# Performance work log

Hardware: AMD Instinct MI355X
Metric: run time of the kernel (lower is better)

## Reference

```python
import jax, jax.numpy as jnp
import numpy as np

N, D, F, E, K = 8192, 1024, 4096, 8, 2


def setup_inputs() -> dict:
    key = jax.random.key(0)
    ks = jax.random.split(key, 4)
    x = jax.random.normal(ks[0], (N, D), dtype=jnp.float32)
    Wg = jax.random.normal(ks[1], (D, E), dtype=jnp.float32) * 0.02
    W1 = jax.random.normal(ks[2], (E, D, F), dtype=jnp.float32) * 0.02
    b1 = jnp.zeros((E, F), dtype=jnp.float32)
    W2 = jax.random.normal(ks[3], (E, F, D), dtype=jnp.float32) * 0.02
    b2 = jnp.zeros((E, D), dtype=jnp.float32)
    return {"x": x, "Wg": Wg, "W1": W1, "b1": b1, "W2": W2, "b2": b2}


def reference(x, Wg, W1, b1, W2, b2):
    # Top-k softmax gate (TopKGate): pick K experts per token, renormalize.
    logits = x @ Wg                                        # [N, E]
    probs = jax.nn.softmax(logits, axis=-1)
    gate_vals, expert_idx = jax.lax.top_k(probs, K)        # [N, K]
    gate_w = gate_vals / jnp.sum(gate_vals, axis=-1, keepdims=True)

    # Expert FFN (dispatch/combine math): the torch code sorts tokens by expert
    # id, all-to-alls them to the owning rank, applies the local Expert MLP,
    # and combines back weighted by gate_w. The jit-friendly equivalent is to
    # compute every expert's MLP for all tokens and gather the selected rows.
    h = jax.nn.relu(jnp.einsum('nd,edf->enf', x, W1) + b1[:, None, :])  # [E, N, F]
    o = jnp.einsum('enf,efd->end', h, W2) + b2[:, None, :]               # [E, N, D]

    tok = jnp.arange(x.shape[0])
    sel = o[expert_idx, tok[:, None]]                      # [N, K, D]
    y = jnp.sum(gate_w[..., None] * sel, axis=1)           # [N, D]
    return y
```

## Files before the change

### kernel.cpp

```cpp
#include <hip/hip_runtime.h>

#define N_TOK 8192
#define DIM   1024
#define FFN   4096
#define NEXP  8
#define TOPK  2
#define NENT  (N_TOK * TOPK)
#define MAXM  20

using short8  = __attribute__((ext_vector_type(8))) short;
using floatx4 = __attribute__((ext_vector_type(4))) float;

__device__ __forceinline__ unsigned short f2bf(float f) {
    union { float f; unsigned u; } v; v.f = f;
    unsigned r = v.u + 0x7fffu + ((v.u >> 16) & 1u);
    return (unsigned short)(r >> 16);
}

#define GLOAD_LDS16(gptr, lptr) __builtin_amdgcn_global_load_lds( \
    (__attribute__((address_space(1))) void*)(void*)(gptr),       \
    (__attribute__((address_space(3))) void*)(lptr), 16, 0, 0)


__global__ __launch_bounds__(256) void cvt_x_kernel(const float4* __restrict__ in,
                                                    ushort4* __restrict__ out) {
    int i = blockIdx.x * 256 + threadIdx.x;
    float4 v = in[i];
    ushort4 o;
    o.x = f2bf(v.x); o.y = f2bf(v.y); o.z = f2bf(v.z); o.w = f2bf(v.w);
    out[i] = o;
}

__global__ __launch_bounds__(256) void transpose_cvt(const float* __restrict__ in,
                                                     unsigned short* __restrict__ out,
                                                     int R, int C) {
    __shared__ float tile[64][65];
    int e  = blockIdx.z;
    int c0 = blockIdx.x * 64;
    int r0 = blockIdx.y * 64;
    const float* inp = in + (size_t)e * R * C;
    unsigned short* outp = out + (size_t)e * R * C;
    int tid = threadIdx.x;
    int lrow = tid >> 6, lcol = tid & 63;
#pragma unroll
    for (int i = 0; i < 16; i++) {
        int r = i * 4 + lrow;
        tile[r][lcol] = inp[(size_t)(r0 + r) * C + c0 + lcol];
    }
    __syncthreads();
    int r4 = (tid & 15) * 4;
#pragma unroll
    for (int i = 0; i < 4; i++) {
        int c = i * 16 + (tid >> 4);
        ushort4 o;
        o.x = f2bf(tile[r4 + 0][c]);
        o.y = f2bf(tile[r4 + 1][c]);
        o.z = f2bf(tile[r4 + 2][c]);
        o.w = f2bf(tile[r4 + 3][c]);
        *(ushort4*)&outp[(size_t)(c0 + c) * R + r0 + r4] = o;
    }
}


__global__ __launch_bounds__(256) void gating_kernel(const float* __restrict__ x,
                                                     const float* __restrict__ wg,
                                                     int* __restrict__ topk_e,
                                                     float* __restrict__ topk_w,
                                                     int* __restrict__ counts) {
    int wave = threadIdx.x >> 6, lane = threadIdx.x & 63;
    int t = blockIdx.x * 4 + wave;
    const float* xr = x + (size_t)t * DIM;
    float acc[NEXP];
#pragma unroll
    for (int e = 0; e < NEXP; e++) acc[e] = 0.f;
    for (int it = 0; it < DIM / 64; it++) {
        int d = it * 64 + lane;
        float xv = xr[d];
        const float4* wr = (const float4*)(wg + d * NEXP);
        float4 w0 = wr[0], w1 = wr[1];
        acc[0] += xv * w0.x; acc[1] += xv * w0.y; acc[2] += xv * w0.z; acc[3] += xv * w0.w;
        acc[4] += xv * w1.x; acc[5] += xv * w1.y; acc[6] += xv * w1.z; acc[7] += xv * w1.w;
    }
#pragma unroll
    for (int e = 0; e < NEXP; e++) {
#pragma unroll
        for (int off = 32; off > 0; off >>= 1) acc[e] += __shfl_xor(acc[e], off);
    }
    if (lane == 0) {
        int e1 = 0; float l1 = acc[0];
        for (int e = 1; e < NEXP; e++) if (acc[e] > l1) { l1 = acc[e]; e1 = e; }
        int e2 = -1; float l2 = -3.4e38f;
        for (int e = 0; e < NEXP; e++) if (e != e1 && acc[e] > l2) { l2 = acc[e]; e2 = e; }
        float w1v = 1.f / (1.f + expf(l2 - l1));
        topk_e[t * 2]     = e1;  topk_e[t * 2 + 1] = e2;
        topk_w[t * 2]     = w1v; topk_w[t * 2 + 1] = 1.f - w1v;
        atomicAdd(&counts[e1], 1);
        atomicAdd(&counts[e2], 1);
    }
}

__global__ void prefix_kernel(const int* __restrict__ counts, int* __restrict__ offs) {
    if (threadIdx.x == 0) {
        int s = 0;
        for (int e = 0; e < NEXP; e++) { offs[e] = s; s += counts[e]; }
        offs[NEXP] = s;
    }
}

__global__ __launch_bounds__(256) void scatter_kernel(const int* __restrict__ topk_e,
                                                      const float* __restrict__ topk_w,
                                                      const int* __restrict__ offs,
                                                      int* __restrict__ cursors,
                                                      int* __restrict__ entry_token,
                                                      float* __restrict__ entry_wgt) {
    int t = blockIdx.x * 256 + threadIdx.x;
#pragma unroll
    for (int k = 0; k < TOPK; k++) {
        int e = topk_e[t * 2 + k];
        int pos = offs[e] + atomicAdd(&cursors[e], 1);
        entry_token[pos] = t;
        entry_wgt[pos]  = topk_w[t * 2 + k];
    }
}


__global__ __launch_bounds__(256) void gemm1_kernel(
    const unsigned short* __restrict__ xb,
    const unsigned short* __restrict__ w1t,
    const float* __restrict__ b1,
    const int* __restrict__ offs,
    const int* __restrict__ entry_token,
    unsigned short* __restrict__ h)
{
    int bid  = blockIdx.x;
    int e    = bid & 7;
    int grp  = bid % (8 * MAXM);
    int mt   = grp >> 3;
    int nt   = bid / (8 * MAXM);
    int base = offs[e];
    int cnt  = offs[e + 1] - base;
    int m0   = mt * 128;
    if (m0 >= cnt) return;
    int f0   = nt * 128;

    __shared__ unsigned short As[128 * 32];
    __shared__ unsigned short Bs[128 * 32];
    __shared__ int toks[128];

    int tid = threadIdx.x;
    if (tid < 128) {
        int r = m0 + tid;
        toks[tid] = entry_token[base + (r < cnt ? r : 0)];
    }
    __syncthreads();

    int wave = tid >> 6, lane = tid & 63;
    int wm = (wave >> 1) * 64, wn = (wave & 1) * 64;

    int lr = lane >> 2, sl = lane & 3;
    int g0 = (sl ^ ((lr >> 1) & 3)) * 8;
    const unsigned short* aG[2];
    const unsigned short* bG[2];
    unsigned short* ldsA[2];
    unsigned short* ldsB[2];
#pragma unroll
    for (int c = 0; c < 2; c++) {
        int row = wave * 32 + c * 16 + lr;
        aG[c] = xb + (size_t)toks[row] * DIM + g0;
        bG[c] = w1t + ((size_t)e * FFN + f0 + row) * DIM + g0;
        ldsA[c] = &As[(wave * 32 + c * 16) * 32];
        ldsB[c] = &Bs[(wave * 32 + c * 16) * 32];
    }

    floatx4 acc[4][4];
#pragma unroll
    for (int i = 0; i < 4; i++)
#pragma unroll
        for (int j = 0; j < 4; j++) acc[i][j] = (floatx4)0.f;

    int quad = lane >> 4, rm = lane & 15;
    int slf  = (quad ^ ((rm >> 1) & 3)) * 8;
    int arow = (wm + rm) * 32;
    int brow = (wn + rm) * 32;

    for (int kk = 0; kk < DIM / 32; kk++) {
        GLOAD_LDS16(aG[0], ldsA[0]);
        GLOAD_LDS16(aG[1], ldsA[1]);
        GLOAD_LDS16(bG[0], ldsB[0]);
        GLOAD_LDS16(bG[1], ldsB[1]);
        aG[0] += 32; aG[1] += 32; bG[0] += 32; bG[1] += 32;
        __syncthreads();
        short8 af[4], bfr[4];
#pragma unroll
        for (int mi = 0; mi < 4; mi++) af[mi] = *(const short8*)&As[arow + mi * 512 + slf];
#pragma unroll
        for (int ni = 0; ni < 4; ni++) bfr[ni] = *(const short8*)&Bs[brow + ni * 512 + slf];
#pragma unroll
        for (int mi = 0; mi < 4; mi++)
#pragma unroll
            for (int ni = 0; ni < 4; ni++)
                acc[mi][ni] = __builtin_amdgcn_mfma_f32_16x16x32_bf16(af[mi], bfr[ni], acc[mi][ni], 0, 0, 0);
        __syncthreads();
    }

#pragma unroll
    for (int mi = 0; mi < 4; mi++) {
        int mbase = wm + mi * 16 + quad * 4;
#pragma unroll
        for (int ni = 0; ni < 4; ni++) {
            int f = f0 + wn + ni * 16 + rm;
            float bias = b1[e * FFN + f];
            floatx4 v = acc[mi][ni];
#pragma unroll
            for (int r = 0; r < 4; r++) {
                int row = m0 + mbase + r;
                if (row < cnt) {
                    float t = v[r] + bias;
                    t = t > 0.f ? t : 0.f;
                    h[(size_t)(base + row) * FFN + f] = f2bf(t);
                }
            }
        }
    }
}


__global__ __launch_bounds__(256) void gemm2_kernel(
    const unsigned short* __restrict__ h,
    const unsigned short* __restrict__ w2t,
    const float* __restrict__ b2,
    const int* __restrict__ offs,
    const int* __restrict__ entry_token,
    const float* __restrict__ entry_wgt,
    float* __restrict__ y)
{
    int bid  = blockIdx.x;
    int e    = bid & 7;
    int grp  = bid % (8 * MAXM);
    int mt   = grp >> 3;
    int nt   = bid / (8 * MAXM);
    int base = offs[e];
    int cnt  = offs[e + 1] - base;
    int m0   = mt * 128;
    if (m0 >= cnt) return;
    int n0   = nt * 128;

    __shared__ unsigned short As[128 * 32];
    __shared__ unsigned short Bs[128 * 32];

    int tid = threadIdx.x;
    int wave = tid >> 6, lane = tid & 63;
    int wm = (wave >> 1) * 64, wn = (wave & 1) * 64;

    int lr = lane >> 2, sl = lane & 3;
    int g0 = (sl ^ ((lr >> 1) & 3)) * 8;
    const unsigned short* aG[2];
    const unsigned short* bG[2];
    unsigned short* ldsA[2];
    unsigned short* ldsB[2];
#pragma unroll
    for (int c = 0; c < 2; c++) {
        int row = wave * 32 + c * 16 + lr;
        aG[c] = h + (size_t)(base + m0 + row) * FFN + g0;
        bG[c] = w2t + ((size_t)e * DIM + n0 + row) * FFN + g0;
        ldsA[c] = &As[(wave * 32 + c * 16) * 32];
        ldsB[c] = &Bs[(wave * 32 + c * 16) * 32];
    }

    floatx4 acc[4][4];
#pragma unroll
    for (int i = 0; i < 4; i++)
#pragma unroll
        for (int j = 0; j < 4; j++) acc[i][j] = (floatx4)0.f;

    int quad = lane >> 4, rm = lane & 15;
    int slf  = (quad ^ ((rm >> 1) & 3)) * 8;
    int arow = (wm + rm) * 32;
    int brow = (wn + rm) * 32;

    for (int kk = 0; kk < FFN / 32; kk++) {
        GLOAD_LDS16(aG[0], ldsA[0]);
        GLOAD_LDS16(aG[1], ldsA[1]);
        GLOAD_LDS16(bG[0], ldsB[0]);
        GLOAD_LDS16(bG[1], ldsB[1]);
        aG[0] += 32; aG[1] += 32; bG[0] += 32; bG[1] += 32;
        __syncthreads();
        short8 af[4], bfr[4];
#pragma unroll
        for (int mi = 0; mi < 4; mi++) af[mi] = *(const short8*)&As[arow + mi * 512 + slf];
#pragma unroll
        for (int ni = 0; ni < 4; ni++) bfr[ni] = *(const short8*)&Bs[brow + ni * 512 + slf];
#pragma unroll
        for (int mi = 0; mi < 4; mi++)
#pragma unroll
            for (int ni = 0; ni < 4; ni++)
                acc[mi][ni] = __builtin_amdgcn_mfma_f32_16x16x32_bf16(af[mi], bfr[ni], acc[mi][ni], 0, 0, 0);
        __syncthreads();
    }

#pragma unroll
    for (int mi = 0; mi < 4; mi++) {
        int mbase = wm + mi * 16 + quad * 4;
#pragma unroll
        for (int ni = 0; ni < 4; ni++) {
            int n = n0 + wn + ni * 16 + rm;
            float bias = b2[e * DIM + n];
            floatx4 v = acc[mi][ni];
#pragma unroll
            for (int r = 0; r < 4; r++) {
                int row = m0 + mbase + r;
                if (row < cnt) {
                    int   tok = entry_token[base + row];
                    float w   = entry_wgt[base + row];
                    atomicAdd(&y[(size_t)tok * DIM + n], (v[r] + bias) * w);
                }
            }
        }
    }
}


extern "C" void kernel_launch(void* const* d_in, const int* in_sizes, int n_in,
                              void* d_out, int out_size, void* d_ws, size_t ws_size,
                              hipStream_t stream) {
    const float* x  = (const float*)d_in[0];
    const float* Wg = (const float*)d_in[1];
    const float* W1 = (const float*)d_in[2];
    const float* b1 = (const float*)d_in[3];
    const float* W2 = (const float*)d_in[4];
    const float* b2 = (const float*)d_in[5];
    float* y = (float*)d_out;

    char* p = (char*)d_ws;
    unsigned short* xb  = (unsigned short*)p; p += (size_t)N_TOK * DIM * 2;
    unsigned short* w1t = (unsigned short*)p; p += (size_t)NEXP * DIM * FFN * 2;
    unsigned short* w2t = (unsigned short*)p; p += (size_t)NEXP * DIM * FFN * 2;
    unsigned short* h   = (unsigned short*)p; p += (size_t)(NENT + 128) * FFN * 2;
    int*   topk_e      = (int*)p;   p += (size_t)N_TOK * TOPK * 4;
    float* topk_w      = (float*)p; p += (size_t)N_TOK * TOPK * 4;
    int*   entry_token = (int*)p;   p += (size_t)NENT * 4;
    float* entry_wgt   = (float*)p; p += (size_t)NENT * 4;
    int*   counts      = (int*)p;   p += NEXP * 4;
    int*   cursors     = (int*)p;   p += NEXP * 4;
    int*   offs        = (int*)p;   p += (NEXP + 1) * 4;

    hipMemsetAsync(d_out, 0, (size_t)out_size * 4, stream);
    hipMemsetAsync(counts, 0, NEXP * 4 * 2, stream);

    cvt_x_kernel<<<(N_TOK * DIM) / (256 * 4), 256, 0, stream>>>((const float4*)x, (ushort4*)xb);
    transpose_cvt<<<dim3(FFN / 64, DIM / 64, NEXP), 256, 0, stream>>>(W1, w1t, DIM, FFN);
    transpose_cvt<<<dim3(DIM / 64, FFN / 64, NEXP), 256, 0, stream>>>(W2, w2t, FFN, DIM);
    gating_kernel<<<N_TOK / 4, 256, 0, stream>>>(x, Wg, topk_e, topk_w, counts);
    prefix_kernel<<<1, 64, 0, stream>>>(counts, offs);
    scatter_kernel<<<N_TOK / 256, 256, 0, stream>>>(topk_e, topk_w, offs, cursors, entry_token, entry_wgt);
    gemm1_kernel<<<NEXP * MAXM * (FFN / 128), 256, 0, stream>>>(xb, w1t, b1, offs, entry_token, h);
    gemm2_kernel<<<NEXP * MAXM * (DIM / 128), 256, 0, stream>>>(h, w2t, b2, offs, entry_token, entry_wgt, y);
}
```

Measured before the change: 1.117 ms.

## Double-buffer LDS in expert GEMMs and replace atomic combine with gather kernel

Both expert GEMMs now double-buffer the A/B tiles in LDS. The next k-slice is issued via global_load_lds before the MFMAs on the current one, and one of the two barriers per iteration is dropped. gemm2 no longer does scattered fp32 atomicAdds into y. It writes bf16 per-entry outputs into the reused w1t buffer, and a new combine kernel gathers each token's two rows and applies the gate weights, which also removes the output memset. The costs are an extra kernel, a bf16 rounding of expert outputs before combining, and occupancy hints of 3 blocks per CU.

```diff
diff --git a/kernel.cpp b/kernel.cpp
--- a/kernel.cpp
+++ b/kernel.cpp
@@ -15,6 +15,11 @@
     union { float f; unsigned u; } v; v.f = f;
     unsigned r = v.u + 0x7fffu + ((v.u >> 16) & 1u);
     return (unsigned short)(r >> 16);
+}
+
+__device__ __forceinline__ float bf2f(unsigned short s) {
+    union { unsigned u; float f; } v; v.u = ((unsigned)s) << 16;
+    return v.f;
 }
 
 #define GLOAD_LDS16(gptr, lptr) __builtin_amdgcn_global_load_lds( \
@@ -112,19 +117,19 @@
                                                       const int* __restrict__ offs,
                                                       int* __restrict__ cursors,
                                                       int* __restrict__ entry_token,
-                                                      float* __restrict__ entry_wgt) {
+                                                      int* __restrict__ entry_pos) {
     int t = blockIdx.x * 256 + threadIdx.x;
 #pragma unroll
     for (int k = 0; k < TOPK; k++) {
         int e = topk_e[t * 2 + k];
         int pos = offs[e] + atomicAdd(&cursors[e], 1);
         entry_token[pos] = t;
-        entry_wgt[pos]  = topk_w[t * 2 + k];
-    }
-}
-
-
-__global__ __launch_bounds__(256) void gemm1_kernel(
+        entry_pos[t * 2 + k] = pos;
+    }
+}
+
+
+__global__ __launch_bounds__(256, 3) void gemm1_kernel(
     const unsigned short* __restrict__ xb,
     const unsigned short* __restrict__ w1t,
     const float* __restrict__ b1,
@@ -143,8 +148,8 @@
     if (m0 >= cnt) return;
     int f0   = nt * 128;
 
-    __shared__ unsigned short As[128 * 32];
-    __shared__ unsigned short Bs[128 * 32];
+    __shared__ unsigned short As[2][128 * 32];
+    __shared__ unsigned short Bs[2][128 * 32];
     __shared__ int toks[128];
 
     int tid = threadIdx.x;
@@ -161,15 +166,13 @@
     int g0 = (sl ^ ((lr >> 1) & 3)) * 8;
     const unsigned short* aG[2];
     const unsigned short* bG[2];
-    unsigned short* ldsA[2];
-    unsigned short* ldsB[2];
+    int ldsOff[2];
 #pragma unroll
     for (int c = 0; c < 2; c++) {
         int row = wave * 32 + c * 16 + lr;
         aG[c] = xb + (size_t)toks[row] * DIM + g0;
         bG[c] = w1t + ((size_t)e * FFN + f0 + row) * DIM + g0;
-        ldsA[c] = &As[(wave * 32 + c * 16) * 32];
-        ldsB[c] = &Bs[(wave * 32 + c * 16) * 32];
+        ldsOff[c] = (wave * 32 + c * 16) * 32;
     }
 
     floatx4 acc[4][4];
@@ -183,24 +186,36 @@
     int arow = (wm + rm) * 32;
     int brow = (wn + rm) * 32;
 
+#pragma unroll
+    for (int c = 0; c < 2; c++) {
+        GLOAD_LDS16(aG[c], &As[0][ldsOff[c]]);
+        GLOAD_LDS16(bG[c], &Bs[0][ldsOff[c]]);
+        aG[c] += 32; bG[c] += 32;
+    }
+
+    int cur = 0;
     for (int kk = 0; kk < DIM / 32; kk++) {
-        GLOAD_LDS16(aG[0], ldsA[0]);
-        GLOAD_LDS16(aG[1], ldsA[1]);
-        GLOAD_LDS16(bG[0], ldsB[0]);
-        GLOAD_LDS16(bG[1], ldsB[1]);
-        aG[0] += 32; aG[1] += 32; bG[0] += 32; bG[1] += 32;
         __syncthreads();
         short8 af[4], bfr[4];
 #pragma unroll
-        for (int mi = 0; mi < 4; mi++) af[mi] = *(const short8*)&As[arow + mi * 512 + slf];
-#pragma unroll
-        for (int ni = 0; ni < 4; ni++) bfr[ni] = *(const short8*)&Bs[brow + ni * 512 + slf];
+        for (int mi = 0; mi < 4; mi++) af[mi] = *(const short8*)&As[cur][arow + mi * 512 + slf];
+#pragma unroll
+        for (int ni = 0; ni < 4; ni++) bfr[ni] = *(const short8*)&Bs[cur][brow + ni * 512 + slf];
+        if (kk + 1 < DIM / 32) {
+            int nxt = cur ^ 1;
+#pragma unroll
+            for (int c = 0; c < 2; c++) {
+                GLOAD_LDS16(aG[c], &As[nxt][ldsOff[c]]);
+                GLOAD_LDS16(bG[c], &Bs[nxt][ldsOff[c]]);
+                aG[c] += 32; bG[c] += 32;
+            }
+        }
 #pragma unroll
         for (int mi = 0; mi < 4; mi++)
 #pragma unroll
             for (int ni = 0; ni < 4; ni++)
                 acc[mi][ni] = __builtin_amdgcn_mfma_f32_16x16x32_bf16(af[mi], bfr[ni], acc[mi][ni], 0, 0, 0);
-        __syncthreads();
+        cur ^= 1;
     }
 
 #pragma unroll
@@ -225,14 +240,12 @@
 }
 
 
-__global__ __launch_bounds__(256) void gemm2_kernel(
+__global__ __launch_bounds__(256, 3) void gemm2_kernel(
     const unsigned short* __restrict__ h,
     const unsigned short* __restrict__ w2t,
     const float* __restrict__ b2,
     const int* __restrict__ offs,
-    const int* __restrict__ entry_token,
-    const float* __restrict__ entry_wgt,
-    float* __restrict__ y)
+    unsigned short* __restrict__ o)
 {
     int bid  = blockIdx.x;
     int e    = bid & 7;
@@ -245,8 +258,8 @@
     if (m0 >= cnt) return;
     int n0   = nt * 128;
 
-    __shared__ unsigned short As[128 * 32];
-    __shared__ unsigned short Bs[128 * 32];
+    __shared__ unsigned short As[2][128 * 32];
+    __shared__ unsigned short Bs[2][128 * 32];
 
     int tid = threadIdx.x;
     int wave = tid >> 6, lane = tid & 63;
@@ -256,15 +269,13 @@
     int g0 = (sl ^ ((lr >> 1) & 3)) * 8;
     const unsigned short* aG[2];
     const unsigned short* bG[2];
-    unsigned short* ldsA[2];
-    unsigned short* ldsB[2];
+    int ldsOff[2];
 #pragma unroll
     for (int c = 0; c < 2; c++) {
         int row = wave * 32 + c * 16 + lr;
         aG[c] = h + (size_t)(base + m0 + row) * FFN + g0;
         bG[c] = w2t + ((size_t)e * DIM + n0 + row) * FFN + g0;
-        ldsA[c] = &As[(wave * 32 + c * 16) * 32];
-        ldsB[c] = &Bs[(wave * 32 + c * 16) * 32];
+        ldsOff[c] = (wave * 32 + c * 16) * 32;
     }
 
     floatx4 acc[4][4];
@@ -278,24 +289,36 @@
     int arow = (wm + rm) * 32;
     int brow = (wn + rm) * 32;
 
+#pragma unroll
+    for (int c = 0; c < 2; c++) {
+        GLOAD_LDS16(aG[c], &As[0][ldsOff[c]]);
+        GLOAD_LDS16(bG[c], &Bs[0][ldsOff[c]]);
+        aG[c] += 32; bG[c] += 32;
+    }
+
+    int cur = 0;
     for (int kk = 0; kk < FFN / 32; kk++) {
-        GLOAD_LDS16(aG[0], ldsA[0]);
-        GLOAD_LDS16(aG[1], ldsA[1]);
-        GLOAD_LDS16(bG[0], ldsB[0]);
-        GLOAD_LDS16(bG[1], ldsB[1]);
-        aG[0] += 32; aG[1] += 32; bG[0] += 32; bG[1] += 32;
         __syncthreads();
         short8 af[4], bfr[4];
 #pragma unroll
-        for (int mi = 0; mi < 4; mi++) af[mi] = *(const short8*)&As[arow + mi * 512 + slf];
-#pragma unroll
-        for (int ni = 0; ni < 4; ni++) bfr[ni] = *(const short8*)&Bs[brow + ni * 512 + slf];
+        for (int mi = 0; mi < 4; mi++) af[mi] = *(const short8*)&As[cur][arow + mi * 512 + slf];
+#pragma unroll
+        for (int ni = 0; ni < 4; ni++) bfr[ni] = *(const short8*)&Bs[cur][brow + ni * 512 + slf];
+        if (kk + 1 < FFN / 32) {
+            int nxt = cur ^ 1;
+#pragma unroll
+            for (int c = 0; c < 2; c++) {
+                GLOAD_LDS16(aG[c], &As[nxt][ldsOff[c]]);
+                GLOAD_LDS16(bG[c], &Bs[nxt][ldsOff[c]]);
+                aG[c] += 32; bG[c] += 32;
+            }
+        }
 #pragma unroll
         for (int mi = 0; mi < 4; mi++)
 #pragma unroll
             for (int ni = 0; ni < 4; ni++)
                 acc[mi][ni] = __builtin_amdgcn_mfma_f32_16x16x32_bf16(af[mi], bfr[ni], acc[mi][ni], 0, 0, 0);
-        __syncthreads();
+        cur ^= 1;
     }
 
 #pragma unroll
@@ -309,14 +332,30 @@
 #pragma unroll
             for (int r = 0; r < 4; r++) {
                 int row = m0 + mbase + r;
-                if (row < cnt) {
-                    int   tok = entry_token[base + row];
-                    float w   = entry_wgt[base + row];
-                    atomicAdd(&y[(size_t)tok * DIM + n], (v[r] + bias) * w);
-                }
+                if (row < cnt)
+                    o[(size_t)(base + row) * DIM + n] = f2bf(v[r] + bias);
             }
         }
     }
+}
+
+
+__global__ __launch_bounds__(256) void combine_kernel(const unsigned short* __restrict__ o,
+                                                      const int* __restrict__ entry_pos,
+                                                      const float* __restrict__ topk_w,
+                                                      float* __restrict__ y) {
+    int t = blockIdx.x;
+    int d = threadIdx.x * 4;
+    int p0 = entry_pos[t * 2], p1 = entry_pos[t * 2 + 1];
+    float w0 = topk_w[t * 2], w1 = topk_w[t * 2 + 1];
+    ushort4 a = *(const ushort4*)&o[(size_t)p0 * DIM + d];
+    ushort4 b = *(const ushort4*)&o[(size_t)p1 * DIM + d];
+    float4 r;
+    r.x = w0 * bf2f(a.x) + w1 * bf2f(b.x);
+    r.y = w0 * bf2f(a.y) + w1 * bf2f(b.y);
+    r.z = w0 * bf2f(a.z) + w1 * bf2f(b.z);
+    r.w = w0 * bf2f(a.w) + w1 * bf2f(b.w);
+    *(float4*)&y[(size_t)t * DIM + d] = r;
 }
 
 
@@ -339,12 +378,13 @@
     int*   topk_e      = (int*)p;   p += (size_t)N_TOK * TOPK * 4;
     float* topk_w      = (float*)p; p += (size_t)N_TOK * TOPK * 4;
     int*   entry_token = (int*)p;   p += (size_t)NENT * 4;
-    float* entry_wgt   = (float*)p; p += (size_t)NENT * 4;
+    int*   entry_pos   = (int*)p;   p += (size_t)NENT * 4;
     int*   counts      = (int*)p;   p += NEXP * 4;
     int*   cursors     = (int*)p;   p += NEXP * 4;
     int*   offs        = (int*)p;   p += (NEXP + 1) * 4;
 
-    hipMemsetAsync(d_out, 0, (size_t)out_size * 4, stream);
+    unsigned short* o = w1t;
+
     hipMemsetAsync(counts, 0, NEXP * 4 * 2, stream);
 
     cvt_x_kernel<<<(N_TOK * DIM) / (256 * 4), 256, 0, stream>>>((const float4*)x, (ushort4*)xb);
@@ -352,7 +392,8 @@
     transpose_cvt<<<dim3(DIM / 64, FFN / 64, NEXP), 256, 0, stream>>>(W2, w2t, FFN, DIM);
     gating_kernel<<<N_TOK / 4, 256, 0, stream>>>(x, Wg, topk_e, topk_w, counts);
     prefix_kernel<<<1, 64, 0, stream>>>(counts, offs);
-    scatter_kernel<<<N_TOK / 256, 256, 0, stream>>>(topk_e, topk_w, offs, cursors, entry_token, entry_wgt);
+    scatter_kernel<<<N_TOK / 256, 256, 0, stream>>>(topk_e, topk_w, offs, cursors, entry_token, entry_pos);
     gemm1_kernel<<<NEXP * MAXM * (FFN / 128), 256, 0, stream>>>(xb, w1t, b1, offs, entry_token, h);
-    gemm2_kernel<<<NEXP * MAXM * (DIM / 128), 256, 0, stream>>>(h, w2t, b2, offs, entry_token, entry_wgt, y);
-}
+    gemm2_kernel<<<NEXP * MAXM * (DIM / 128), 256, 0, stream>>>(h, w2t, b2, offs, o);
+    combine_kernel<<<N_TOK, 256, 0, stream>>>(o, entry_pos, topk_w, y);
+}
```

Result: faster. 1.056 ms (-5.4%).
